# Kernel tuning notes

Hardware: AMD Instinct MI355X
Metric: run time of the kernel (lower is better)

The kernel has to match this reference:

```python
import jax, jax.numpy as jnp
import numpy as np

N_NODES = 50000
N_EDGES = 800000
D = 128


def setup_inputs() -> dict:
    key = jax.random.key(0)
    k1, k2, k3, k4 = jax.random.split(key, 4)
    x1 = jax.random.normal(k1, (N_NODES, D), dtype=jnp.float32)
    adj = jax.random.randint(k2, (2, N_EDGES), 0, N_NODES, dtype=jnp.int64)
    scale = 1.0 / np.sqrt(D)
    W1 = jax.random.normal(k3, (D, D), dtype=jnp.float32) * scale
    b1 = jnp.zeros((D,), dtype=jnp.float32)
    W2 = jax.random.normal(k4, (D, D), dtype=jnp.float32) * scale
    b2 = jnp.zeros((D,), dtype=jnp.float32)
    return {"x1": x1, "adj": adj, "W1": W1, "b1": b1, "W2": W2, "b2": b2}


def reference(x1, adj, W1, b1, W2, b2):
    num_nodes = x1.shape[0]
    # message: gather source-node features per edge -> [E, D]
    edge_x = x1[adj[0]]
    # aggregate: scatter-max into destination nodes -> [N, D]
    x2 = jax.ops.segment_max(edge_x, adj[1], num_segments=num_nodes)
    # empty segments yield -inf; torch_scatter fills them with 0
    x2 = jnp.where(jnp.isneginf(x2), jnp.zeros_like(x2), x2)
    # combine: residual add + 2-layer MLP
    h = jax.nn.relu((x1 + x2) @ W1 + b1)
    return h @ W2 + b2
```

## Files before the change

kernel.cpp:

```cpp
#include <hip/hip_runtime.h>
#include <stdint.h>
#include <math.h>

#define DD 128
#define ROWS 128
#define CAP 64

typedef unsigned short u16;
typedef unsigned int   u32;
typedef __attribute__((ext_vector_type(8))) short bf16x8;
typedef __attribute__((ext_vector_type(4))) float f32x4;

__device__ __forceinline__ u16 f2bf(float f) {
    u32 u = __float_as_uint(f);
    return (u16)((u + 0x7fffu + ((u >> 16) & 1u)) >> 16);
}
__device__ __forceinline__ float bf_lo(u32 u) { return __uint_as_float(u << 16); }
__device__ __forceinline__ float bf_hi(u32 u) { return __uint_as_float(u & 0xffff0000u); }

__device__ __forceinline__ int swz(int row, int byte_in_row) {
    return row * 256 + (byte_in_row ^ ((row & 7) << 4));
}

__global__ __launch_bounds__(256) void fill_cvt_w_k(
    const int* __restrict__ adj, int* __restrict__ deg,
    u16* __restrict__ ent,
    const float* __restrict__ x1, u16* __restrict__ x1bf,
    const float* __restrict__ W1, const float* __restrict__ W2,
    u16* __restrict__ W1T, u16* __restrict__ W2T,
    int n_edges, int n_nodes)
{
    if ((int)blockIdx.x == (int)gridDim.x - 1) {
        for (int t = threadIdx.x; t < 4096; t += 256) {
            int m = t >> 11;
            int idx = t & 2047;
            int c = idx >> 4, k8 = idx & 15;
            const float* W = m ? W2 : W1;
            u16* WT = m ? W2T : W1T;
            u16 tmp[8];
            #pragma unroll
            for (int j = 0; j < 8; ++j) tmp[j] = f2bf(W[(k8 * 8 + j) * DD + c]);
            uint4 v;
            v.x = (u32)tmp[0] | ((u32)tmp[1] << 16);
            v.y = (u32)tmp[2] | ((u32)tmp[3] << 16);
            v.z = (u32)tmp[4] | ((u32)tmp[5] << 16);
            v.w = (u32)tmp[6] | ((u32)tmp[7] << 16);
            *(uint4*)((char*)WT + swz(c, k8 * 16)) = v;
        }
        return;
    }
    int t = blockIdx.x * 256 + threadIdx.x;

    if (t < n_edges) {
        int src = adj[t];
        int dst = adj[n_edges + t];
        if ((unsigned)src < (unsigned)n_nodes && (unsigned)dst < (unsigned)n_nodes) {
            int slot = atomicAdd(&deg[dst], 1);
            if (slot < CAP) ent[(size_t)dst * CAP + slot] = (u16)src;
        }
    }

    int n_cvt = n_nodes * 16;
    if (t < n_cvt) {
        const float4* x4 = (const float4*)x1;
        float4 a = x4[(size_t)t * 2];
        float4 b = x4[(size_t)t * 2 + 1];
        uint4 v;
        v.x = (u32)f2bf(a.x) | ((u32)f2bf(a.y) << 16);
        v.y = (u32)f2bf(a.z) | ((u32)f2bf(a.w) << 16);
        v.z = (u32)f2bf(b.x) | ((u32)f2bf(b.y) << 16);
        v.w = (u32)f2bf(b.z) | ((u32)f2bf(b.w) << 16);
        ((uint4*)x1bf)[t] = v;
    }
}

__global__ __launch_bounds__(256) void gather_max_k(
    const u16* __restrict__ x1bf, const int* __restrict__ deg,
    const u16* __restrict__ ent, u16* __restrict__ xin, int n_nodes)
{
    int node = blockIdx.x * 16 + (threadIdx.x >> 4);
    int q = threadIdx.x & 15;
    if (node >= n_nodes) return;
    int d = deg[node];
    if (d > CAP) d = CAP;
    const u16* en = ent + (size_t)node * CAP;
    const uint4* xb = (const uint4*)x1bf;

    float m[4][8];
    #pragma unroll
    for (int j = 0; j < 4; ++j)
        #pragma unroll
        for (int k = 0; k < 8; ++k) m[j][k] = -INFINITY;

    int i = 0;
    for (; i + 3 < d; i += 4) {
        uint2 e4 = *(const uint2*)(en + i);
        int s0 = e4.x & 0xffff, s1 = e4.x >> 16;
        int s2 = e4.y & 0xffff, s3 = e4.y >> 16;
        uint4 v0 = xb[(size_t)s0 * 16 + q];
        uint4 v1 = xb[(size_t)s1 * 16 + q];
        uint4 v2 = xb[(size_t)s2 * 16 + q];
        uint4 v3 = xb[(size_t)s3 * 16 + q];
        #define ACC(J, V) \
            m[J][0]=fmaxf(m[J][0],bf_lo(V.x)); m[J][1]=fmaxf(m[J][1],bf_hi(V.x)); \
            m[J][2]=fmaxf(m[J][2],bf_lo(V.y)); m[J][3]=fmaxf(m[J][3],bf_hi(V.y)); \
            m[J][4]=fmaxf(m[J][4],bf_lo(V.z)); m[J][5]=fmaxf(m[J][5],bf_hi(V.z)); \
            m[J][6]=fmaxf(m[J][6],bf_lo(V.w)); m[J][7]=fmaxf(m[J][7],bf_hi(V.w));
        ACC(0, v0) ACC(1, v1) ACC(2, v2) ACC(3, v3)
    }
    for (; i < d; ++i) {
        int s0 = en[i];
        uint4 v0 = xb[(size_t)s0 * 16 + q];
        ACC(0, v0)
        #undef ACC
    }
    #pragma unroll
    for (int k = 0; k < 8; ++k)
        m[0][k] = fmaxf(fmaxf(m[0][k], m[1][k]), fmaxf(m[2][k], m[3][k]));

    uint4 sv = xb[(size_t)node * 16 + q];
    float r[8];
    r[0]=bf_lo(sv.x); r[1]=bf_hi(sv.x); r[2]=bf_lo(sv.y); r[3]=bf_hi(sv.y);
    r[4]=bf_lo(sv.z); r[5]=bf_hi(sv.z); r[6]=bf_lo(sv.w); r[7]=bf_hi(sv.w);
    if (d > 0) {
        #pragma unroll
        for (int k = 0; k < 8; ++k) r[k] += m[0][k];
    }
    uint4 o;
    o.x = (u32)f2bf(r[0]) | ((u32)f2bf(r[1]) << 16);
    o.y = (u32)f2bf(r[2]) | ((u32)f2bf(r[3]) << 16);
    o.z = (u32)f2bf(r[4]) | ((u32)f2bf(r[5]) << 16);
    o.w = (u32)f2bf(r[6]) | ((u32)f2bf(r[7]) << 16);
    ((uint4*)xin)[(size_t)node * 16 + q] = o;
}

__global__ __launch_bounds__(256, 2) void mlp_mfma_k(
    const u16* __restrict__ xin,
    const u16* __restrict__ W1T, const float* __restrict__ b1,
    const u16* __restrict__ W2T, const float* __restrict__ b2,
    float* __restrict__ out, int n_rows)
{
    __shared__ uint4 sXq[ROWS * 16];
    __shared__ uint4 sWq[128 * 16];
    char* sX = (char*)sXq;
    char* sW = (char*)sWq;

    const int tid  = threadIdx.x;
    const int wave = tid >> 6;
    const int lane = tid & 63;
    const int lhi  = lane >> 4, llo = lane & 15;
    const int row0 = blockIdx.x * ROWS;

    {
        const uint4* src = (const uint4*)xin;
        #pragma unroll
        for (int i = tid; i < ROWS * 16; i += 256) {
            int r = i >> 4, c8 = i & 15;
            uint4 v = make_uint4(0, 0, 0, 0);
            if (row0 + r < n_rows) v = src[(size_t)(row0 + r) * 16 + c8];
            *(uint4*)(sX + swz(r, c8 * 16)) = v;
        }
        const uint4* wsrc = (const uint4*)W1T;
        #pragma unroll
        for (int i = tid; i < 2048; i += 256) sWq[i] = wsrc[i];
    }
    __syncthreads();

    const int wrow0 = wave * 32;

    f32x4 acc[2][8];
    #pragma unroll
    for (int mi = 0; mi < 2; ++mi)
        #pragma unroll
        for (int nj = 0; nj < 8; ++nj)
            acc[mi][nj] = (f32x4){0.f, 0.f, 0.f, 0.f};

    #pragma unroll
    for (int kstep = 0; kstep < 4; ++kstep) {
        int kb = (kstep * 32 + lhi * 8) * 2;
        int ra = wrow0 + llo, rb = wrow0 + 16 + llo;
        bf16x8 a0 = *(const bf16x8*)(sX + swz(ra, kb));
        bf16x8 a1 = *(const bf16x8*)(sX + swz(rb, kb));
        #pragma unroll
        for (int nj = 0; nj < 8; ++nj) {
            int c = nj * 16 + llo;
            bf16x8 b = *(const bf16x8*)(sW + swz(c, kb));
            acc[0][nj] = __builtin_amdgcn_mfma_f32_16x16x32_bf16(a0, b, acc[0][nj], 0, 0, 0);
            acc[1][nj] = __builtin_amdgcn_mfma_f32_16x16x32_bf16(a1, b, acc[1][nj], 0, 0, 0);
        }
    }

    #pragma unroll
    for (int nj = 0; nj < 8; ++nj) {
        int col = nj * 16 + llo;
        float bv = b1[col];
        #pragma unroll
        for (int mi = 0; mi < 2; ++mi) {
            #pragma unroll
            for (int r = 0; r < 4; ++r) {
                int row = wrow0 + mi * 16 + lhi * 4 + r;
                float h = fmaxf(acc[mi][nj][r] + bv, 0.f);
                *(u16*)(sX + swz(row, col * 2)) = f2bf(h);
            }
        }
    }
    __syncthreads();

    {
        const uint4* wsrc = (const uint4*)W2T;
        #pragma unroll
        for (int i = tid; i < 2048; i += 256) sWq[i] = wsrc[i];
    }
    __syncthreads();

    #pragma unroll
    for (int mi = 0; mi < 2; ++mi)
        #pragma unroll
        for (int nj = 0; nj < 8; ++nj)
            acc[mi][nj] = (f32x4){0.f, 0.f, 0.f, 0.f};

    #pragma unroll
    for (int kstep = 0; kstep < 4; ++kstep) {
        int kb = (kstep * 32 + lhi * 8) * 2;
        int ra = wrow0 + llo, rb = wrow0 + 16 + llo;
        bf16x8 a0 = *(const bf16x8*)(sX + swz(ra, kb));
        bf16x8 a1 = *(const bf16x8*)(sX + swz(rb, kb));
        #pragma unroll
        for (int nj = 0; nj < 8; ++nj) {
            int c = nj * 16 + llo;
            bf16x8 b = *(const bf16x8*)(sW + swz(c, kb));
            acc[0][nj] = __builtin_amdgcn_mfma_f32_16x16x32_bf16(a0, b, acc[0][nj], 0, 0, 0);
            acc[1][nj] = __builtin_amdgcn_mfma_f32_16x16x32_bf16(a1, b, acc[1][nj], 0, 0, 0);
        }
    }

    #pragma unroll
    for (int nj = 0; nj < 8; ++nj) {
        int col = nj * 16 + llo;
        float bv = b2[col];
        #pragma unroll
        for (int mi = 0; mi < 2; ++mi) {
            #pragma unroll
            for (int r = 0; r < 4; ++r) {
                int row = row0 + wrow0 + mi * 16 + lhi * 4 + r;
                if (row < n_rows)
                    out[(size_t)row * DD + col] = acc[mi][nj][r] + bv;
            }
        }
    }
}

extern "C" void kernel_launch(void* const* d_in, const int* in_sizes, int n_in,
                              void* d_out, int out_size, void* d_ws, size_t ws_size,
                              hipStream_t stream) {
    const float* x1  = (const float*)d_in[0];
    const int*   adj = (const int*)d_in[1];
    const float* W1  = (const float*)d_in[2];
    const float* b1  = (const float*)d_in[3];
    const float* W2  = (const float*)d_in[4];
    const float* b2  = (const float*)d_in[5];
    float* out = (float*)d_out;

    const int n_nodes = in_sizes[0] / DD;
    const int n_edges = in_sizes[1] / 2;

    u16* x1bf = (u16*)d_out;

    char* ws = (char*)d_ws;
    size_t off = 0;
    u16* xin = (u16*)(ws + off); off += (size_t)n_nodes * DD * sizeof(u16);
    u16* ent = (u16*)(ws + off); off += (size_t)n_nodes * CAP * sizeof(u16);
    u16* W1T = (u16*)(ws + off); off += (size_t)DD * DD * sizeof(u16);
    u16* W2T = (u16*)(ws + off); off += (size_t)DD * DD * sizeof(u16);
    int* deg = (int*)(ws + off); off += (size_t)n_nodes * sizeof(int);

    hipMemsetAsync(deg, 0, (size_t)n_nodes * sizeof(int), stream);

    int eb = (n_edges + 255) / 256;
    fill_cvt_w_k<<<eb + 1, 256, 0, stream>>>(adj, deg, ent, x1, x1bf,
                                             W1, W2, W1T, W2T, n_edges, n_nodes);

    gather_max_k<<<(n_nodes + 15) / 16, 256, 0, stream>>>(x1bf, deg, ent, xin, n_nodes);
    mlp_mfma_k<<<(n_nodes + ROWS - 1) / ROWS, 256, 0, stream>>>(
        xin, W1T, b1, W2T, b2, out, n_nodes);
}
```

Before: 120.2 us.

## Replace per-node global atomic bucketing with two-level group binning in shared memory

Edge bucketing by destination now runs in two stages instead of one global atomic and scattered 2-byte write per edge. A binning kernel sorts chunks of edges into 64-node groups in LDS and writes them contiguously into per-group regions. The gather kernel then builds the per-node adjacency lists for its group in shared memory before doing the max-gather. The aim is to cut global atomic contention and the scattered writes to the 6.4MB ent table, in exchange for an extra kernel launch, a fixed per-group capacity (REGCAP 2048) that can silently drop edges, and large LDS use in binA.

```diff
diff --git a/kernel.cpp b/kernel.cpp
--- a/kernel.cpp
+++ b/kernel.cpp
@@ -5,6 +5,12 @@
 #define DD 128
 #define ROWS 128
 #define CAP 64
+#define GBITS 6
+#define GSZ 64
+#define NGMAX 1024
+#define CHUNK 8192
+#define RPT (CHUNK/256)
+#define REGCAP 2048
 
 typedef unsigned short u16;
 typedef unsigned int   u32;
@@ -22,13 +28,10 @@
     return row * 256 + (byte_in_row ^ ((row & 7) << 4));
 }
 
-__global__ __launch_bounds__(256) void fill_cvt_w_k(
-    const int* __restrict__ adj, int* __restrict__ deg,
-    u16* __restrict__ ent,
+__global__ __launch_bounds__(256) void cvt_w_k(
     const float* __restrict__ x1, u16* __restrict__ x1bf,
     const float* __restrict__ W1, const float* __restrict__ W2,
-    u16* __restrict__ W1T, u16* __restrict__ W2T,
-    int n_edges, int n_nodes)
+    u16* __restrict__ W1T, u16* __restrict__ W2T, int n_nodes)
 {
     if ((int)blockIdx.x == (int)gridDim.x - 1) {
         for (int t = threadIdx.x; t < 4096; t += 256) {
@@ -50,16 +53,6 @@
         return;
     }
     int t = blockIdx.x * 256 + threadIdx.x;
-
-    if (t < n_edges) {
-        int src = adj[t];
-        int dst = adj[n_edges + t];
-        if ((unsigned)src < (unsigned)n_nodes && (unsigned)dst < (unsigned)n_nodes) {
-            int slot = atomicAdd(&deg[dst], 1);
-            if (slot < CAP) ent[(size_t)dst * CAP + slot] = (u16)src;
-        }
-    }
-
     int n_cvt = n_nodes * 16;
     if (t < n_cvt) {
         const float4* x4 = (const float4*)x1;
@@ -74,64 +67,173 @@
     }
 }
 
-__global__ __launch_bounds__(256) void gather_max_k(
-    const u16* __restrict__ x1bf, const int* __restrict__ deg,
-    const u16* __restrict__ ent, u16* __restrict__ xin, int n_nodes)
+__global__ __launch_bounds__(256) void binA_k(
+    const int* __restrict__ adj, int* __restrict__ gcur,
+    u32* __restrict__ region, int n_edges, int n_nodes, int n_groups)
 {
-    int node = blockIdx.x * 16 + (threadIdx.x >> 4);
-    int q = threadIdx.x & 15;
-    if (node >= n_nodes) return;
-    int d = deg[node];
-    if (d > CAP) d = CAP;
-    const u16* en = ent + (size_t)node * CAP;
+    __shared__ int cnt[NGMAX];
+    __shared__ int start[NGMAX];
+    __shared__ int baseg[NGMAX];
+    __shared__ int wsum[4];
+    __shared__ u32 ls[CHUNK];
+
+    const int tid = threadIdx.x;
+    const int wid = tid >> 6, lane = tid & 63;
+    const int chunk0 = blockIdx.x * CHUNK;
+    const int nrec = min(CHUNK, n_edges - chunk0);
+
+    for (int i = tid; i < n_groups; i += 256) cnt[i] = 0;
+    __syncthreads();
+
+    u32 rec[RPT], br[RPT];
+    #pragma unroll
+    for (int r = 0; r < RPT; ++r) {
+        int idx = r * 256 + tid;
+        u32 record = 0, binrank = 0xffffffffu;
+        if (idx < nrec) {
+            int e = chunk0 + idx;
+            int src = adj[e];
+            int dst = adj[n_edges + e];
+            if ((unsigned)src < (unsigned)n_nodes && (unsigned)dst < (unsigned)n_nodes) {
+                int g = dst >> GBITS;
+                int rank = atomicAdd(&cnt[g], 1);
+                record  = ((u32)(dst & (GSZ - 1)) << 16) | (u32)src;
+                binrank = ((u32)g << 16) | (u32)rank;
+            }
+        }
+        rec[r] = record; br[r] = binrank;
+    }
+    __syncthreads();
+
+    {
+        int b4 = tid * 4;
+        int s0 = (b4 + 0 < n_groups) ? cnt[b4 + 0] : 0;
+        int s1 = (b4 + 1 < n_groups) ? cnt[b4 + 1] : 0;
+        int s2 = (b4 + 2 < n_groups) ? cnt[b4 + 2] : 0;
+        int s3 = (b4 + 3 < n_groups) ? cnt[b4 + 3] : 0;
+        int tsum = s0 + s1 + s2 + s3;
+        int incl = tsum;
+        #pragma unroll
+        for (int off = 1; off < 64; off <<= 1) {
+            int t = __shfl_up(incl, off);
+            if (lane >= off) incl += t;
+        }
+        if (lane == 63) wsum[wid] = incl;
+        __syncthreads();
+        int woff = 0;
+        #pragma unroll
+        for (int j = 0; j < 4; ++j) if (j < wid) woff += wsum[j];
+        int excl = woff + incl - tsum;
+        if (b4 + 0 < n_groups) start[b4 + 0] = excl;
+        if (b4 + 1 < n_groups) start[b4 + 1] = excl + s0;
+        if (b4 + 2 < n_groups) start[b4 + 2] = excl + s0 + s1;
+        if (b4 + 3 < n_groups) start[b4 + 3] = excl + s0 + s1 + s2;
+    }
+    for (int g = tid; g < n_groups; g += 256)
+        baseg[g] = atomicAdd(&gcur[g], cnt[g]);
+    __syncthreads();
+
+    #pragma unroll
+    for (int r = 0; r < RPT; ++r) {
+        if (br[r] != 0xffffffffu) {
+            int g = br[r] >> 16, rank = br[r] & 0xffff;
+            ls[start[g] + rank] = rec[r];
+        }
+    }
+    __syncthreads();
+
+    for (int g = wid; g < n_groups; g += 4) {
+        int c = cnt[g], st = start[g], bg = baseg[g];
+        u32* dstp = region + (size_t)g * REGCAP;
+        for (int i = lane; i < c; i += 64) {
+            int slot = bg + i;
+            if (slot < REGCAP) dstp[slot] = ls[st + i];
+        }
+    }
+}
+
+__global__ __launch_bounds__(256) void bucket_gather_k(
+    const u16* __restrict__ x1bf, const int* __restrict__ gcur,
+    const u32* __restrict__ region, u16* __restrict__ xin, int n_nodes)
+{
+    __shared__ int deg_l[GSZ];
+    __shared__ u16 ent_l[GSZ * CAP];
+
+    const int g = blockIdx.x;
+    const int tid = threadIdx.x;
+    const int node0 = g << GBITS;
+
+    for (int i = tid; i < GSZ; i += 256) deg_l[i] = 0;
+    __syncthreads();
+
+    int cnt = min(gcur[g], REGCAP);
+    const u32* rp = region + (size_t)g * REGCAP;
+    for (int i = tid; i < cnt; i += 256) {
+        u32 rc = rp[i];
+        int l = rc >> 16, src = rc & 0xffff;
+        int slot = atomicAdd(&deg_l[l], 1);
+        if (slot < CAP) ent_l[(l << 6) + slot] = (u16)src;
+    }
+    __syncthreads();
+
     const uint4* xb = (const uint4*)x1bf;
-
-    float m[4][8];
-    #pragma unroll
-    for (int j = 0; j < 4; ++j)
-        #pragma unroll
-        for (int k = 0; k < 8; ++k) m[j][k] = -INFINITY;
-
-    int i = 0;
-    for (; i + 3 < d; i += 4) {
-        uint2 e4 = *(const uint2*)(en + i);
-        int s0 = e4.x & 0xffff, s1 = e4.x >> 16;
-        int s2 = e4.y & 0xffff, s3 = e4.y >> 16;
-        uint4 v0 = xb[(size_t)s0 * 16 + q];
-        uint4 v1 = xb[(size_t)s1 * 16 + q];
-        uint4 v2 = xb[(size_t)s2 * 16 + q];
-        uint4 v3 = xb[(size_t)s3 * 16 + q];
-        #define ACC(J, V) \
-            m[J][0]=fmaxf(m[J][0],bf_lo(V.x)); m[J][1]=fmaxf(m[J][1],bf_hi(V.x)); \
-            m[J][2]=fmaxf(m[J][2],bf_lo(V.y)); m[J][3]=fmaxf(m[J][3],bf_hi(V.y)); \
-            m[J][4]=fmaxf(m[J][4],bf_lo(V.z)); m[J][5]=fmaxf(m[J][5],bf_hi(V.z)); \
-            m[J][6]=fmaxf(m[J][6],bf_lo(V.w)); m[J][7]=fmaxf(m[J][7],bf_hi(V.w));
-        ACC(0, v0) ACC(1, v1) ACC(2, v2) ACC(3, v3)
-    }
-    for (; i < d; ++i) {
-        int s0 = en[i];
-        uint4 v0 = xb[(size_t)s0 * 16 + q];
-        ACC(0, v0)
-        #undef ACC
-    }
-    #pragma unroll
-    for (int k = 0; k < 8; ++k)
-        m[0][k] = fmaxf(fmaxf(m[0][k], m[1][k]), fmaxf(m[2][k], m[3][k]));
-
-    uint4 sv = xb[(size_t)node * 16 + q];
-    float r[8];
-    r[0]=bf_lo(sv.x); r[1]=bf_hi(sv.x); r[2]=bf_lo(sv.y); r[3]=bf_hi(sv.y);
-    r[4]=bf_lo(sv.z); r[5]=bf_hi(sv.z); r[6]=bf_lo(sv.w); r[7]=bf_hi(sv.w);
-    if (d > 0) {
-        #pragma unroll
-        for (int k = 0; k < 8; ++k) r[k] += m[0][k];
-    }
-    uint4 o;
-    o.x = (u32)f2bf(r[0]) | ((u32)f2bf(r[1]) << 16);
-    o.y = (u32)f2bf(r[2]) | ((u32)f2bf(r[3]) << 16);
-    o.z = (u32)f2bf(r[4]) | ((u32)f2bf(r[5]) << 16);
-    o.w = (u32)f2bf(r[6]) | ((u32)f2bf(r[7]) << 16);
-    ((uint4*)xin)[(size_t)node * 16 + q] = o;
+    const int q = tid & 15;
+
+    #pragma unroll
+    for (int it = 0; it < 4; ++it) {
+        int l = it * 16 + (tid >> 4);
+        int node = node0 + l;
+        if (node >= n_nodes) continue;
+        int d = min(deg_l[l], CAP);
+        const u16* en = &ent_l[l << 6];
+
+        float m[4][8];
+        #pragma unroll
+        for (int j = 0; j < 4; ++j)
+            #pragma unroll
+            for (int k = 0; k < 8; ++k) m[j][k] = -INFINITY;
+
+        int i = 0;
+        for (; i + 3 < d; i += 4) {
+            uint2 e4 = *(const uint2*)(en + i);
+            int s0 = e4.x & 0xffff, s1 = e4.x >> 16;
+            int s2 = e4.y & 0xffff, s3 = e4.y >> 16;
+            uint4 v0 = xb[(size_t)s0 * 16 + q];
+            uint4 v1 = xb[(size_t)s1 * 16 + q];
+            uint4 v2 = xb[(size_t)s2 * 16 + q];
+            uint4 v3 = xb[(size_t)s3 * 16 + q];
+            #define ACC(J, V) \
+                m[J][0]=fmaxf(m[J][0],bf_lo(V.x)); m[J][1]=fmaxf(m[J][1],bf_hi(V.x)); \
+                m[J][2]=fmaxf(m[J][2],bf_lo(V.y)); m[J][3]=fmaxf(m[J][3],bf_hi(V.y)); \
+                m[J][4]=fmaxf(m[J][4],bf_lo(V.z)); m[J][5]=fmaxf(m[J][5],bf_hi(V.z)); \
+                m[J][6]=fmaxf(m[J][6],bf_lo(V.w)); m[J][7]=fmaxf(m[J][7],bf_hi(V.w));
+            ACC(0, v0) ACC(1, v1) ACC(2, v2) ACC(3, v3)
+        }
+        for (; i < d; ++i) {
+            int s0 = en[i];
+            uint4 v0 = xb[(size_t)s0 * 16 + q];
+            ACC(0, v0)
+            #undef ACC
+        }
+        #pragma unroll
+        for (int k = 0; k < 8; ++k)
+            m[0][k] = fmaxf(fmaxf(m[0][k], m[1][k]), fmaxf(m[2][k], m[3][k]));
+
+        uint4 sv = xb[(size_t)node * 16 + q];
+        float r[8];
+        r[0]=bf_lo(sv.x); r[1]=bf_hi(sv.x); r[2]=bf_lo(sv.y); r[3]=bf_hi(sv.y);
+        r[4]=bf_lo(sv.z); r[5]=bf_hi(sv.z); r[6]=bf_lo(sv.w); r[7]=bf_hi(sv.w);
+        if (d > 0) {
+            #pragma unroll
+            for (int k = 0; k < 8; ++k) r[k] += m[0][k];
+        }
+        uint4 o;
+        o.x = (u32)f2bf(r[0]) | ((u32)f2bf(r[1]) << 16);
+        o.y = (u32)f2bf(r[2]) | ((u32)f2bf(r[3]) << 16);
+        o.z = (u32)f2bf(r[4]) | ((u32)f2bf(r[5]) << 16);
+        o.w = (u32)f2bf(r[6]) | ((u32)f2bf(r[7]) << 16);
+        ((uint4*)xin)[(size_t)node * 16 + q] = o;
+    }
 }
 
 __global__ __launch_bounds__(256, 2) void mlp_mfma_k(
@@ -263,24 +365,28 @@
 
     const int n_nodes = in_sizes[0] / DD;
     const int n_edges = in_sizes[1] / 2;
+    const int n_groups = (n_nodes + GSZ - 1) / GSZ;
 
     u16* x1bf = (u16*)d_out;
 
     char* ws = (char*)d_ws;
     size_t off = 0;
-    u16* xin = (u16*)(ws + off); off += (size_t)n_nodes * DD * sizeof(u16);
-    u16* ent = (u16*)(ws + off); off += (size_t)n_nodes * CAP * sizeof(u16);
-    u16* W1T = (u16*)(ws + off); off += (size_t)DD * DD * sizeof(u16);
-    u16* W2T = (u16*)(ws + off); off += (size_t)DD * DD * sizeof(u16);
-    int* deg = (int*)(ws + off); off += (size_t)n_nodes * sizeof(int);
-
-    hipMemsetAsync(deg, 0, (size_t)n_nodes * sizeof(int), stream);
-
-    int eb = (n_edges + 255) / 256;
-    fill_cvt_w_k<<<eb + 1, 256, 0, stream>>>(adj, deg, ent, x1, x1bf,
-                                             W1, W2, W1T, W2T, n_edges, n_nodes);
-
-    gather_max_k<<<(n_nodes + 15) / 16, 256, 0, stream>>>(x1bf, deg, ent, xin, n_nodes);
+    u16* xin    = (u16*)(ws + off); off += (size_t)n_nodes * DD * sizeof(u16);
+    u32* region = (u32*)(ws + off); off += (size_t)n_groups * REGCAP * sizeof(u32);
+    u16* W1T    = (u16*)(ws + off); off += (size_t)DD * DD * sizeof(u16);
+    u16* W2T    = (u16*)(ws + off); off += (size_t)DD * DD * sizeof(u16);
+    int* gcur   = (int*)(ws + off); off += (size_t)n_groups * sizeof(int);
+
+    hipMemsetAsync(gcur, 0, (size_t)n_groups * sizeof(int), stream);
+
+    int ncvt_blk = (n_nodes * 16 + 255) / 256;
+    cvt_w_k<<<ncvt_blk + 1, 256, 0, stream>>>(x1, x1bf, W1, W2, W1T, W2T, n_nodes);
+
+    int na_blk = (n_edges + CHUNK - 1) / CHUNK;
+    binA_k<<<na_blk, 256, 0, stream>>>(adj, gcur, region, n_edges, n_nodes, n_groups);
+
+    bucket_gather_k<<<n_groups, 256, 0, stream>>>(x1bf, gcur, region, xin, n_nodes);
+
     mlp_mfma_k<<<(n_nodes + ROWS - 1) / ROWS, 256, 0, stream>>>(
         xin, W1T, b1, W2T, b2, out, n_nodes);
 }
```

Result: slower. 141.6 us (+17.8%).

## Split edge fill by destination half and overlap second fill with first-half gather

Applied to the files above, without the earlier changes.

Splits edge bucketing into two passes by destination range. The first pass handles destinations in the lower half, fused with the bf16 conversion. The second pass, for the upper half, runs in the same launch as the max-gather for the lower half, then a third kernel gathers the upper half. The goal is to hide gather latency behind the atomic fill work. The cost is reading the adjacency array twice and adding one kernel launch.

```diff
diff --git a/kernel.cpp b/kernel.cpp
--- a/kernel.cpp
+++ b/kernel.cpp
@@ -22,13 +22,86 @@
     return row * 256 + (byte_in_row ^ ((row & 7) << 4));
 }
 
-__global__ __launch_bounds__(256) void fill_cvt_w_k(
-    const int* __restrict__ adj, int* __restrict__ deg,
-    u16* __restrict__ ent,
+
+__device__ __forceinline__ void do_fill(
+    const int* __restrict__ adj, int* __restrict__ deg, u16* __restrict__ ent,
+    int n_edges, int n_nodes, int lo, int hi, int t)
+{
+    if (t < n_edges) {
+        int src = adj[t];
+        int dst = adj[n_edges + t];
+        if ((unsigned)src < (unsigned)n_nodes && dst >= lo && dst < hi) {
+            int slot = atomicAdd(&deg[dst], 1);
+            if (slot < CAP) ent[(size_t)dst * CAP + slot] = (u16)src;
+        }
+    }
+}
+
+__device__ __forceinline__ void do_gather(
+    const u16* __restrict__ x1bf, const int* __restrict__ deg,
+    const u16* __restrict__ ent, u16* __restrict__ xin,
+    int node, int q, int n_nodes)
+{
+    if (node >= n_nodes) return;
+    int d = deg[node];
+    if (d > CAP) d = CAP;
+    const u16* en = ent + (size_t)node * CAP;
+    const uint4* xb = (const uint4*)x1bf;
+
+    float m[4][8];
+    #pragma unroll
+    for (int j = 0; j < 4; ++j)
+        #pragma unroll
+        for (int k = 0; k < 8; ++k) m[j][k] = -INFINITY;
+
+    int i = 0;
+    for (; i + 3 < d; i += 4) {
+        uint2 e4 = *(const uint2*)(en + i);
+        int s0 = e4.x & 0xffff, s1 = e4.x >> 16;
+        int s2 = e4.y & 0xffff, s3 = e4.y >> 16;
+        uint4 v0 = xb[(size_t)s0 * 16 + q];
+        uint4 v1 = xb[(size_t)s1 * 16 + q];
+        uint4 v2 = xb[(size_t)s2 * 16 + q];
+        uint4 v3 = xb[(size_t)s3 * 16 + q];
+        #define ACC(J, V) \
+            m[J][0]=fmaxf(m[J][0],bf_lo(V.x)); m[J][1]=fmaxf(m[J][1],bf_hi(V.x)); \
+            m[J][2]=fmaxf(m[J][2],bf_lo(V.y)); m[J][3]=fmaxf(m[J][3],bf_hi(V.y)); \
+            m[J][4]=fmaxf(m[J][4],bf_lo(V.z)); m[J][5]=fmaxf(m[J][5],bf_hi(V.z)); \
+            m[J][6]=fmaxf(m[J][6],bf_lo(V.w)); m[J][7]=fmaxf(m[J][7],bf_hi(V.w));
+        ACC(0, v0) ACC(1, v1) ACC(2, v2) ACC(3, v3)
+    }
+    for (; i < d; ++i) {
+        int s0 = en[i];
+        uint4 v0 = xb[(size_t)s0 * 16 + q];
+        ACC(0, v0)
+        #undef ACC
+    }
+    #pragma unroll
+    for (int k = 0; k < 8; ++k)
+        m[0][k] = fmaxf(fmaxf(m[0][k], m[1][k]), fmaxf(m[2][k], m[3][k]));
+
+    uint4 sv = xb[(size_t)node * 16 + q];
+    float r[8];
+    r[0]=bf_lo(sv.x); r[1]=bf_hi(sv.x); r[2]=bf_lo(sv.y); r[3]=bf_hi(sv.y);
+    r[4]=bf_lo(sv.z); r[5]=bf_hi(sv.z); r[6]=bf_lo(sv.w); r[7]=bf_hi(sv.w);
+    if (d > 0) {
+        #pragma unroll
+        for (int k = 0; k < 8; ++k) r[k] += m[0][k];
+    }
+    uint4 o;
+    o.x = (u32)f2bf(r[0]) | ((u32)f2bf(r[1]) << 16);
+    o.y = (u32)f2bf(r[2]) | ((u32)f2bf(r[3]) << 16);
+    o.z = (u32)f2bf(r[4]) | ((u32)f2bf(r[5]) << 16);
+    o.w = (u32)f2bf(r[6]) | ((u32)f2bf(r[7]) << 16);
+    ((uint4*)xin)[(size_t)node * 16 + q] = o;
+}
+
+__global__ __launch_bounds__(256) void fillA_cvt_w_k(
+    const int* __restrict__ adj, int* __restrict__ deg, u16* __restrict__ ent,
     const float* __restrict__ x1, u16* __restrict__ x1bf,
     const float* __restrict__ W1, const float* __restrict__ W2,
     u16* __restrict__ W1T, u16* __restrict__ W2T,
-    int n_edges, int n_nodes)
+    int n_edges, int n_nodes, int H)
 {
     if ((int)blockIdx.x == (int)gridDim.x - 1) {
         for (int t = threadIdx.x; t < 4096; t += 256) {
@@ -50,15 +123,7 @@
         return;
     }
     int t = blockIdx.x * 256 + threadIdx.x;
-
-    if (t < n_edges) {
-        int src = adj[t];
-        int dst = adj[n_edges + t];
-        if ((unsigned)src < (unsigned)n_nodes && (unsigned)dst < (unsigned)n_nodes) {
-            int slot = atomicAdd(&deg[dst], 1);
-            if (slot < CAP) ent[(size_t)dst * CAP + slot] = (u16)src;
-        }
-    }
+    do_fill(adj, deg, ent, n_edges, n_nodes, 0, H, t);
 
     int n_cvt = n_nodes * 16;
     if (t < n_cvt) {
@@ -74,64 +139,28 @@
     }
 }
 
-__global__ __launch_bounds__(256) void gather_max_k(
+__global__ __launch_bounds__(256) void fillB_gatherA_k(
+    const int* __restrict__ adj, int* __restrict__ deg, u16* __restrict__ ent,
+    const u16* __restrict__ x1bf, u16* __restrict__ xin,
+    int n_edges, int n_nodes, int H, int eb)
+{
+    if ((int)blockIdx.x < eb) {
+        int t = blockIdx.x * 256 + threadIdx.x;
+        do_fill(adj, deg, ent, n_edges, n_nodes, H, n_nodes, t);
+        return;
+    }
+    int gb = blockIdx.x - eb;
+    int node = gb * 16 + (threadIdx.x >> 4);
+    if (node >= H) return;
+    do_gather(x1bf, deg, ent, xin, node, threadIdx.x & 15, n_nodes);
+}
+
+__global__ __launch_bounds__(256) void gatherB_k(
     const u16* __restrict__ x1bf, const int* __restrict__ deg,
-    const u16* __restrict__ ent, u16* __restrict__ xin, int n_nodes)
-{
-    int node = blockIdx.x * 16 + (threadIdx.x >> 4);
-    int q = threadIdx.x & 15;
-    if (node >= n_nodes) return;
-    int d = deg[node];
-    if (d > CAP) d = CAP;
-    const u16* en = ent + (size_t)node * CAP;
-    const uint4* xb = (const uint4*)x1bf;
-
-    float m[4][8];
-    #pragma unroll
-    for (int j = 0; j < 4; ++j)
-        #pragma unroll
-        for (int k = 0; k < 8; ++k) m[j][k] = -INFINITY;
-
-    int i = 0;
-    for (; i + 3 < d; i += 4) {
-        uint2 e4 = *(const uint2*)(en + i);
-        int s0 = e4.x & 0xffff, s1 = e4.x >> 16;
-        int s2 = e4.y & 0xffff, s3 = e4.y >> 16;
-        uint4 v0 = xb[(size_t)s0 * 16 + q];
-        uint4 v1 = xb[(size_t)s1 * 16 + q];
-        uint4 v2 = xb[(size_t)s2 * 16 + q];
-        uint4 v3 = xb[(size_t)s3 * 16 + q];
-        #define ACC(J, V) \
-            m[J][0]=fmaxf(m[J][0],bf_lo(V.x)); m[J][1]=fmaxf(m[J][1],bf_hi(V.x)); \
-            m[J][2]=fmaxf(m[J][2],bf_lo(V.y)); m[J][3]=fmaxf(m[J][3],bf_hi(V.y)); \
-            m[J][4]=fmaxf(m[J][4],bf_lo(V.z)); m[J][5]=fmaxf(m[J][5],bf_hi(V.z)); \
-            m[J][6]=fmaxf(m[J][6],bf_lo(V.w)); m[J][7]=fmaxf(m[J][7],bf_hi(V.w));
-        ACC(0, v0) ACC(1, v1) ACC(2, v2) ACC(3, v3)
-    }
-    for (; i < d; ++i) {
-        int s0 = en[i];
-        uint4 v0 = xb[(size_t)s0 * 16 + q];
-        ACC(0, v0)
-        #undef ACC
-    }
-    #pragma unroll
-    for (int k = 0; k < 8; ++k)
-        m[0][k] = fmaxf(fmaxf(m[0][k], m[1][k]), fmaxf(m[2][k], m[3][k]));
-
-    uint4 sv = xb[(size_t)node * 16 + q];
-    float r[8];
-    r[0]=bf_lo(sv.x); r[1]=bf_hi(sv.x); r[2]=bf_lo(sv.y); r[3]=bf_hi(sv.y);
-    r[4]=bf_lo(sv.z); r[5]=bf_hi(sv.z); r[6]=bf_lo(sv.w); r[7]=bf_hi(sv.w);
-    if (d > 0) {
-        #pragma unroll
-        for (int k = 0; k < 8; ++k) r[k] += m[0][k];
-    }
-    uint4 o;
-    o.x = (u32)f2bf(r[0]) | ((u32)f2bf(r[1]) << 16);
-    o.y = (u32)f2bf(r[2]) | ((u32)f2bf(r[3]) << 16);
-    o.z = (u32)f2bf(r[4]) | ((u32)f2bf(r[5]) << 16);
-    o.w = (u32)f2bf(r[6]) | ((u32)f2bf(r[7]) << 16);
-    ((uint4*)xin)[(size_t)node * 16 + q] = o;
+    const u16* __restrict__ ent, u16* __restrict__ xin, int n_nodes, int H)
+{
+    int node = H + blockIdx.x * 16 + (threadIdx.x >> 4);
+    do_gather(x1bf, deg, ent, xin, node, threadIdx.x & 15, n_nodes);
 }
 
 __global__ __launch_bounds__(256, 2) void mlp_mfma_k(
@@ -263,6 +292,7 @@
 
     const int n_nodes = in_sizes[0] / DD;
     const int n_edges = in_sizes[1] / 2;
+    const int H = n_nodes / 2;
 
     u16* x1bf = (u16*)d_out;
 
@@ -277,10 +307,17 @@
     hipMemsetAsync(deg, 0, (size_t)n_nodes * sizeof(int), stream);
 
     int eb = (n_edges + 255) / 256;
-    fill_cvt_w_k<<<eb + 1, 256, 0, stream>>>(adj, deg, ent, x1, x1bf,
-                                             W1, W2, W1T, W2T, n_edges, n_nodes);
-
-    gather_max_k<<<(n_nodes + 15) / 16, 256, 0, stream>>>(x1bf, deg, ent, xin, n_nodes);
+    fillA_cvt_w_k<<<eb + 1, 256, 0, stream>>>(adj, deg, ent, x1, x1bf,
+                                              W1, W2, W1T, W2T,
+                                              n_edges, n_nodes, H);
+
+    int gaB = (H + 15) / 16;
+    fillB_gatherA_k<<<eb + gaB, 256, 0, stream>>>(adj, deg, ent, x1bf, xin,
+                                                  n_edges, n_nodes, H, eb);
+
+    int gbB = ((n_nodes - H) + 15) / 16;
+    gatherB_k<<<gbB, 256, 0, stream>>>(x1bf, deg, ent, xin, n_nodes, H);
+
     mlp_mfma_k<<<(n_nodes + ROWS - 1) / ROWS, 256, 0, stream>>>(
         xin, W1T, b1, W2T, b2, out, n_nodes);
 }
```

Result: slower. 124.8 us (+3.9%).

## Replace capped per-node edge buckets with 8-way linked lists via atomicExch

Applied to the files above, without the earlier changes.

Edge bucketing changes from a fixed-capacity (CAP=64) per-node u16 slot array filled by atomicAdd to per-node linked lists. Each node has 8 head pointers updated with atomicExch, and each edge record packs its source index and the next pointer. The gather kernel then walks 4 lists at a time, which removes the degree cap and the scattered u16 slot writes and spreads atomic contention over 8 heads. In exchange it adds dependent pointer-chasing loads, whose latency serialises the traversal, and a larger memset of the head array.

```diff
diff --git a/kernel.cpp b/kernel.cpp
--- a/kernel.cpp
+++ b/kernel.cpp
@@ -4,10 +4,11 @@
 
 #define DD 128
 #define ROWS 128
-#define CAP 64
+#define NREP 8
 
 typedef unsigned short u16;
 typedef unsigned int   u32;
+typedef unsigned long long u64;
 typedef __attribute__((ext_vector_type(8))) short bf16x8;
 typedef __attribute__((ext_vector_type(4))) float f32x4;
 
@@ -23,8 +24,7 @@
 }
 
 __global__ __launch_bounds__(256) void fill_cvt_w_k(
-    const int* __restrict__ adj, int* __restrict__ deg,
-    u16* __restrict__ ent,
+    const int* __restrict__ adj, int* __restrict__ head, u64* __restrict__ rec,
     const float* __restrict__ x1, u16* __restrict__ x1bf,
     const float* __restrict__ W1, const float* __restrict__ W2,
     u16* __restrict__ W1T, u16* __restrict__ W2T,
@@ -55,8 +55,8 @@
         int src = adj[t];
         int dst = adj[n_edges + t];
         if ((unsigned)src < (unsigned)n_nodes && (unsigned)dst < (unsigned)n_nodes) {
-            int slot = atomicAdd(&deg[dst], 1);
-            if (slot < CAP) ent[(size_t)dst * CAP + slot] = (u16)src;
+            int old = atomicExch(&head[dst * NREP + (t & (NREP - 1))], t);
+            rec[t] = ((u64)(u32)src << 32) | (u32)old;
         }
     }
 
@@ -75,56 +75,68 @@
 }
 
 __global__ __launch_bounds__(256) void gather_max_k(
-    const u16* __restrict__ x1bf, const int* __restrict__ deg,
-    const u16* __restrict__ ent, u16* __restrict__ xin, int n_nodes)
+    const u16* __restrict__ x1bf, const int* __restrict__ head,
+    const u64* __restrict__ rec, u16* __restrict__ xin, int n_nodes)
 {
     int node = blockIdx.x * 16 + (threadIdx.x >> 4);
     int q = threadIdx.x & 15;
     if (node >= n_nodes) return;
-    int d = deg[node];
-    if (d > CAP) d = CAP;
-    const u16* en = ent + (size_t)node * CAP;
+    const int* hp = head + (size_t)node * NREP;
     const uint4* xb = (const uint4*)x1bf;
 
-    float m[4][8];
-    #pragma unroll
-    for (int j = 0; j < 4; ++j)
-        #pragma unroll
-        for (int k = 0; k < 8; ++k) m[j][k] = -INFINITY;
-
-    int i = 0;
-    for (; i + 3 < d; i += 4) {
-        uint2 e4 = *(const uint2*)(en + i);
-        int s0 = e4.x & 0xffff, s1 = e4.x >> 16;
-        int s2 = e4.y & 0xffff, s3 = e4.y >> 16;
-        uint4 v0 = xb[(size_t)s0 * 16 + q];
-        uint4 v1 = xb[(size_t)s1 * 16 + q];
-        uint4 v2 = xb[(size_t)s2 * 16 + q];
-        uint4 v3 = xb[(size_t)s3 * 16 + q];
-        #define ACC(J, V) \
-            m[J][0]=fmaxf(m[J][0],bf_lo(V.x)); m[J][1]=fmaxf(m[J][1],bf_hi(V.x)); \
-            m[J][2]=fmaxf(m[J][2],bf_lo(V.y)); m[J][3]=fmaxf(m[J][3],bf_hi(V.y)); \
-            m[J][4]=fmaxf(m[J][4],bf_lo(V.z)); m[J][5]=fmaxf(m[J][5],bf_hi(V.z)); \
-            m[J][6]=fmaxf(m[J][6],bf_lo(V.w)); m[J][7]=fmaxf(m[J][7],bf_hi(V.w));
-        ACC(0, v0) ACC(1, v1) ACC(2, v2) ACC(3, v3)
-    }
-    for (; i < d; ++i) {
-        int s0 = en[i];
-        uint4 v0 = xb[(size_t)s0 * 16 + q];
-        ACC(0, v0)
-        #undef ACC
-    }
-    #pragma unroll
-    for (int k = 0; k < 8; ++k)
-        m[0][k] = fmaxf(fmaxf(m[0][k], m[1][k]), fmaxf(m[2][k], m[3][k]));
+    float m[8];
+    #pragma unroll
+    for (int k = 0; k < 8; ++k) m[k] = -INFINITY;
+
+    int h0 = hp[0], h1 = hp[1], h2 = hp[2], h3 = hp[3];
+    int h4 = hp[4], h5 = hp[5], h6 = hp[6], h7 = hp[7];
+    bool has = (h0 & h1 & h2 & h3 & h4 & h5 & h6 & h7) != -1;
+
+    #define ACC(V) \
+        m[0]=fmaxf(m[0],bf_lo(V.x)); m[1]=fmaxf(m[1],bf_hi(V.x)); \
+        m[2]=fmaxf(m[2],bf_lo(V.y)); m[3]=fmaxf(m[3],bf_hi(V.y)); \
+        m[4]=fmaxf(m[4],bf_lo(V.z)); m[5]=fmaxf(m[5],bf_hi(V.z)); \
+        m[6]=fmaxf(m[6],bf_lo(V.w)); m[7]=fmaxf(m[7],bf_hi(V.w));
+
+    #pragma unroll
+    for (int g = 0; g < 2; ++g) {
+        int a = (g == 0) ? h0 : h4;
+        int b = (g == 0) ? h1 : h5;
+        int c = (g == 0) ? h2 : h6;
+        int d = (g == 0) ? h3 : h7;
+        while (a >= 0 || b >= 0 || c >= 0 || d >= 0) {
+            u64 ra = 0, rb = 0, rc = 0, rd = 0;
+            if (a >= 0) ra = rec[a];
+            if (b >= 0) rb = rec[b];
+            if (c >= 0) rc = rec[c];
+            if (d >= 0) rd = rec[d];
+            if (a >= 0) {
+                uint4 v = xb[(size_t)(u32)(ra >> 32) * 16 + q];
+                ACC(v); a = (int)(u32)ra;
+            }
+            if (b >= 0) {
+                uint4 v = xb[(size_t)(u32)(rb >> 32) * 16 + q];
+                ACC(v); b = (int)(u32)rb;
+            }
+            if (c >= 0) {
+                uint4 v = xb[(size_t)(u32)(rc >> 32) * 16 + q];
+                ACC(v); c = (int)(u32)rc;
+            }
+            if (d >= 0) {
+                uint4 v = xb[(size_t)(u32)(rd >> 32) * 16 + q];
+                ACC(v); d = (int)(u32)rd;
+            }
+        }
+    }
+    #undef ACC
 
     uint4 sv = xb[(size_t)node * 16 + q];
     float r[8];
     r[0]=bf_lo(sv.x); r[1]=bf_hi(sv.x); r[2]=bf_lo(sv.y); r[3]=bf_hi(sv.y);
     r[4]=bf_lo(sv.z); r[5]=bf_hi(sv.z); r[6]=bf_lo(sv.w); r[7]=bf_hi(sv.w);
-    if (d > 0) {
-        #pragma unroll
-        for (int k = 0; k < 8; ++k) r[k] += m[0][k];
+    if (has) {
+        #pragma unroll
+        for (int k = 0; k < 8; ++k) r[k] += m[k];
     }
     uint4 o;
     o.x = (u32)f2bf(r[0]) | ((u32)f2bf(r[1]) << 16);
@@ -268,19 +280,19 @@
 
     char* ws = (char*)d_ws;
     size_t off = 0;
-    u16* xin = (u16*)(ws + off); off += (size_t)n_nodes * DD * sizeof(u16);
-    u16* ent = (u16*)(ws + off); off += (size_t)n_nodes * CAP * sizeof(u16);
-    u16* W1T = (u16*)(ws + off); off += (size_t)DD * DD * sizeof(u16);
-    u16* W2T = (u16*)(ws + off); off += (size_t)DD * DD * sizeof(u16);
-    int* deg = (int*)(ws + off); off += (size_t)n_nodes * sizeof(int);
-
-    hipMemsetAsync(deg, 0, (size_t)n_nodes * sizeof(int), stream);
+    u16* xin  = (u16*)(ws + off); off += (size_t)n_nodes * DD * sizeof(u16);
+    u64* rec  = (u64*)(ws + off); off += (size_t)n_edges * sizeof(u64);
+    u16* W1T  = (u16*)(ws + off); off += (size_t)DD * DD * sizeof(u16);
+    u16* W2T  = (u16*)(ws + off); off += (size_t)DD * DD * sizeof(u16);
+    int* head = (int*)(ws + off); off += (size_t)n_nodes * NREP * sizeof(int);
+
+    hipMemsetAsync(head, 0xFF, (size_t)n_nodes * NREP * sizeof(int), stream);
 
     int eb = (n_edges + 255) / 256;
-    fill_cvt_w_k<<<eb + 1, 256, 0, stream>>>(adj, deg, ent, x1, x1bf,
+    fill_cvt_w_k<<<eb + 1, 256, 0, stream>>>(adj, head, rec, x1, x1bf,
                                              W1, W2, W1T, W2T, n_edges, n_nodes);
 
-    gather_max_k<<<(n_nodes + 15) / 16, 256, 0, stream>>>(x1bf, deg, ent, xin, n_nodes);
+    gather_max_k<<<(n_nodes + 15) / 16, 256, 0, stream>>>(x1bf, head, rec, xin, n_nodes);
     mlp_mfma_k<<<(n_nodes + ROWS - 1) / ROWS, 256, 0, stream>>>(
         xin, W1T, b1, W2T, b2, out, n_nodes);
 }
```

New measurement: 123.5 us. 2.8% more time.
